# Performance work log

Measured on AMD Instinct MI355X. Metric: run time of the kernel, lower is better.

The kernel has to match this reference:

```python
import jax, jax.numpy as jnp
import numpy as np

# Module hyperparameters (init_kwargs)
OUTLINER_RATIO = 0.01
SUB_RATIO = 0.2
SUB_BIT = 8
RANK = 16


def setup_inputs() -> dict:
    key = jax.random.key(0)
    x = jax.random.normal(key, (8, 2048, 4096), dtype=jnp.float32)
    return {"x": x}


def _lowrank_approx(A, q, key):
    """Randomized rank-q approximation of A (torch.svd_lowrank style, niter=2).
    A: [N, D]. Returns Q @ (Q^T A), a rank-q approximation of A."""
    n = A.shape[1]
    omega = jax.random.normal(key, (n, q), dtype=A.dtype)
    Q, _ = jnp.linalg.qr(A @ omega)            # [N, q]
    for _ in range(2):                          # power iterations
        Q2, _ = jnp.linalg.qr(A.T @ Q)          # [D, q]
        Q, _ = jnp.linalg.qr(A @ Q2)            # [N, q]
    return Q @ (Q.T @ A)                        # [N, D], rank q


def _get_statistics(x):
    """Outlier threshold (1-ratio quantile of |x[0]|), top-norm column list,
    and per-tensor symmetric quantization scale for the sub-outlier columns."""
    ax0 = jnp.abs(x[0]).ravel()
    k = int(ax0.shape[0] * (1.0 - OUTLINER_RATIO))      # kthvalue, 1-indexed
    outliner = jnp.sort(ax0)[k - 1]
    col_norm = jnp.mean(jnp.abs(x), axis=(0, 1))        # [D] per-column mean |x|
    kcols = int(x.shape[-1] * SUB_RATIO)
    _, cols = jax.lax.top_k(col_norm, kcols)            # sub-outlier column ids
    col_mask = jnp.zeros((x.shape[-1],), bool).at[cols].set(True)
    x_rem = jnp.where(jnp.abs(x) > outliner, 0.0, x)    # remove outliers
    x_sub = jnp.where(col_mask, x_rem, 0.0)
    qmax = float(2 ** (SUB_BIT - 1) - 1)
    scale = jnp.max(jnp.abs(x_sub)) / qmax
    return outliner, cols, scale


def _compress(x, outliner, cols, scale):
    """fake_divide_outliner_suboutlinear_svd: split x into outliers (kept exact),
    sub-outlier columns (fake-quantized to SUB_BIT bits), and a rank-RANK
    approximation of the remainder; recombine."""
    shape = x.shape
    D = shape[-1]
    x_out = jnp.where(jnp.abs(x) > outliner, x, 0.0)
    x_rem = x - x_out
    col_mask = jnp.zeros((D,), bool).at[cols].set(True)
    x_sub = jnp.where(col_mask, x_rem, 0.0)
    x_rem2 = x_rem - x_sub
    qmax = 2 ** (SUB_BIT - 1) - 1
    x_sub_q = jnp.clip(jnp.round(x_sub / scale), -qmax - 1, qmax) * scale
    x_lr = _lowrank_approx(x_rem2.reshape(-1, D), RANK, jax.random.key(42))
    return x_lr.reshape(shape) + x_out + x_sub_q


def reference(x):
    # forward output of the module is exact-erf GELU (F.gelu default)
    result = jax.nn.gelu(x, approximate=False)
    # iteration=0 < 10: compute statistics and the compressed activation
    # that would be saved for backward (this is the custom-kernel-heavy path).
    outliner, cols, scale = _get_statistics(x)
    x_compressed = _compress(x, outliner, cols, scale)
    return result, x_compressed, outliner, scale
```

## Files before the change

### kernel.cpp

```cpp
#include <hip/hip_runtime.h>
#include <math.h>

#define D_   4096
#define N_   16384
#define TOT  67108864ULL
#define KSEL 8304721u

__device__ unsigned long long g_colsum[D_];
__device__ unsigned int  g_hist[2048];
__device__ unsigned int  g_state[2];
__device__ float         g_outliner;
__device__ unsigned int  g_maxbits;
__device__ float         g_scale;
__device__ unsigned char g_mask[D_];
__device__ float g_omega[D_ * 16];
__device__ float g_tall [N_ * 16];
__device__ float g_small[D_ * 16];
__device__ float g_part [16777216];
__device__ float g_gpart[64 * 256];
__device__ float g_M[256];

__device__ __forceinline__ unsigned rotl32(unsigned v, int s) { return (v << s) | (v >> (32 - s)); }

__device__ __forceinline__ float erfinv32(float xx) {
  float w = -log1pf(-xx * xx);
  float p;
  if (w < 5.f) {
    w -= 2.5f;
    p = 2.81022636e-08f;
    p = fmaf(p, w, 3.43273939e-07f);
    p = fmaf(p, w, -3.5233877e-06f);
    p = fmaf(p, w, -4.39150654e-06f);
    p = fmaf(p, w, 0.00021858087f);
    p = fmaf(p, w, -0.00125372503f);
    p = fmaf(p, w, -0.00417768164f);
    p = fmaf(p, w, 0.246640727f);
    p = fmaf(p, w, 1.50140941f);
  } else {
    w = sqrtf(w) - 3.f;
    p = -0.000200214257f;
    p = fmaf(p, w, 0.000100950558f);
    p = fmaf(p, w, 0.00134934322f);
    p = fmaf(p, w, -0.00367342844f);
    p = fmaf(p, w, 0.00573950773f);
    p = fmaf(p, w, -0.0076224613f);
    p = fmaf(p, w, 0.00943887047f);
    p = fmaf(p, w, 1.00167406f);
    p = fmaf(p, w, 2.83297682f);
  }
  return p * xx;
}

__device__ __forceinline__ float bits_to_normal(unsigned b) {
  float f = __uint_as_float((b >> 9) | 0x3f800000u) - 1.0f;
  float u = fmaf(f, 2.0f, -0.99999994f);
  u = fmaxf(-0.99999994f, u);
  return 1.41421356f * erfinv32(u);
}

__device__ __forceinline__ float gelu_exact(float v) {
  return 0.5f * v * (1.f + erff(v * 0.70710678f));
}

__global__ void k_init() {
  int t = threadIdx.x;
  for (int i = t; i < D_; i += 256) g_colsum[i] = 0ull;
  for (int i = t; i < 2048; i += 256) g_hist[i] = 0u;
  if (t == 0) { g_state[0] = KSEL; g_state[1] = 0u; g_maxbits = 0u; }
}

__global__ __launch_bounds__(256) void k_pass1(const float* __restrict__ x, float* __restrict__ out0) {
  __shared__ unsigned lh[4 * 2056];
  int t = threadIdx.x, b = blockIdx.x;
  bool doh = (b < 64);
  for (int i = t; i < 4 * 2056; i += 256) lh[i] = 0u;
  int cp = (t >> 6) * 2056;
  float acc[16];
#pragma unroll
  for (int j = 0; j < 16; ++j) acc[j] = 0.f;
  __syncthreads();
  const float4* xv = (const float4*)(x + (size_t)b * 131072);
  float4* ov = (float4*)(out0 + (size_t)b * 131072);
  for (int i = 0; i < 128; i += 4) {
#pragma unroll
    for (int jj = 0; jj < 4; ++jj) {
      int f = t + 256 * (i + jj);
      float4 v = xv[f];
      float4 g;
      g.x = gelu_exact(v.x); g.y = gelu_exact(v.y); g.z = gelu_exact(v.z); g.w = gelu_exact(v.w);
      ov[f] = g;
      acc[jj * 4 + 0] += fabsf(v.x);
      acc[jj * 4 + 1] += fabsf(v.y);
      acc[jj * 4 + 2] += fabsf(v.z);
      acc[jj * 4 + 3] += fabsf(v.w);
      if (doh) {
        atomicAdd(&lh[cp + ((__float_as_uint(v.x) & 0x7fffffffu) >> 21)], 1u);
        atomicAdd(&lh[cp + ((__float_as_uint(v.y) & 0x7fffffffu) >> 21)], 1u);
        atomicAdd(&lh[cp + ((__float_as_uint(v.z) & 0x7fffffffu) >> 21)], 1u);
        atomicAdd(&lh[cp + ((__float_as_uint(v.w) & 0x7fffffffu) >> 21)], 1u);
      }
    }
  }
#pragma unroll
  for (int jj = 0; jj < 4; ++jj) {
    int c4 = t + 256 * jj;
#pragma unroll
    for (int k = 0; k < 4; ++k) {
      unsigned long long q = (unsigned long long)((double)acc[jj * 4 + k] * 4294967296.0 + 0.5);
      atomicAdd(&g_colsum[4 * c4 + k], q);
    }
  }
  if (doh) {
    __syncthreads();
    for (int i = t; i < 2048; i += 256) {
      unsigned c = lh[i] + lh[2056 + i] + lh[4112 + i] + lh[6168 + i];
      if (c) atomicAdd(&g_hist[i], c);
    }
  }
}

__global__ __launch_bounds__(256) void k_histL(const float* __restrict__ x, int level) {
  __shared__ unsigned lh[2048];
  int t = threadIdx.x, b = blockIdx.x;
  for (int i = t; i < 2048; i += 256) lh[i] = 0u;
  __syncthreads();
  unsigned pre = g_state[1];
  const float4* xv = (const float4*)x;
  size_t base = (size_t)b * 16384;
  for (int i = 0; i < 64; ++i) {
    float4 v = xv[base + t + 256 * i];
    unsigned u;
#define HPROC(comp) \
    u = __float_as_uint(comp) & 0x7fffffffu; \
    if (level == 1) { if ((u >> 21) == (pre >> 21)) atomicAdd(&lh[(u >> 10) & 0x7ffu], 1u); } \
    else            { if ((u >> 10) == (pre >> 10)) atomicAdd(&lh[u & 0x3ffu], 1u); }
    HPROC(v.x) HPROC(v.y) HPROC(v.z) HPROC(v.w)
#undef HPROC
  }
  __syncthreads();
  for (int i = t; i < 2048; i += 256) { unsigned c = lh[i]; if (c) atomicAdd(&g_hist[i], c); }
}

__global__ void k_scan(int level, float* __restrict__ od) {
  __shared__ unsigned h[2048];
  __shared__ unsigned ps[256];
  int t = threadIdx.x;
  unsigned loc = 0;
#pragma unroll
  for (int i = 0; i < 8; ++i) { unsigned v = g_hist[t * 8 + i]; h[t * 8 + i] = v; loc += v; }
  ps[t] = loc;
  __syncthreads();
  if (t == 0) {
    unsigned krem = g_state[0], pre = g_state[1];
    unsigned cum = 0; int g = 0;
    for (; g < 255; ++g) { if (cum + ps[g] >= krem) break; cum += ps[g]; }
    int b = g * 8;
    for (; b < 2047; ++b) { if (cum + h[b] >= krem) break; cum += h[b]; }
    krem -= cum;
    if (level == 0)      pre = ((unsigned)b) << 21;
    else if (level == 1) pre |= ((unsigned)b) << 10;
    else { pre |= (unsigned)b; g_outliner = __uint_as_float(pre); od[0] = __uint_as_float(pre); }
    g_state[0] = krem; g_state[1] = pre;
  }
  __syncthreads();
  for (int i = t; i < 2048; i += 256) g_hist[i] = 0u;
}

__global__ __launch_bounds__(1024) void k_colsel() {
  __shared__ unsigned long long s[4096];
  int t = threadIdx.x;
  for (int m = 0; m < 4; ++m) s[t + 1024 * m] = g_colsum[t + 1024 * m];
  __syncthreads();
  for (int k = 2; k <= 4096; k <<= 1) {
    for (int j = k >> 1; j > 0; j >>= 1) {
#pragma unroll
      for (int m = 0; m < 4; ++m) {
        int i = t + 1024 * m;
        int l = i ^ j;
        if (l > i) {
          unsigned long long a = s[i], c = s[l];
          bool up = ((i & k) == 0);
          if (up ? (a > c) : (a < c)) { s[i] = c; s[l] = a; }
        }
      }
      __syncthreads();
    }
  }
  unsigned long long T = s[4096 - 819];
  for (int m = 0; m < 4; ++m) { int i = t + 1024 * m; g_mask[i] = (g_colsum[i] >= T) ? 1 : 0; }
}

__global__ void k_omega() {
  unsigned i = blockIdx.x * 256 + threadIdx.x;
  if (i >= 65536u) return;
  const unsigned ks0 = 0u, ks1 = 42u, ks2 = 0x1BD11BDAu ^ 42u;
  unsigned x0 = 0u + ks0;
  unsigned x1 = i  + ks1;
#define RND(r) { x0 += x1; x1 = rotl32(x1, r); x1 ^= x0; }
  RND(13) RND(15) RND(26) RND(6)   x0 += ks1; x1 += ks2 + 1u;
  RND(17) RND(29) RND(16) RND(24)  x0 += ks2; x1 += ks0 + 2u;
  RND(13) RND(15) RND(26) RND(6)   x0 += ks0; x1 += ks1 + 3u;
  RND(17) RND(29) RND(16) RND(24)  x0 += ks1; x1 += ks2 + 4u;
  RND(13) RND(15) RND(26) RND(6)   x0 += ks2; x1 += ks0 + 5u;
#undef RND
  g_omega[i] = bits_to_normal(x0 ^ x1);
}

__global__ __launch_bounds__(256) void k_AB(const float* __restrict__ x, int bsel) {
  __shared__ float xt[256 * 33];
  int t = threadIdx.x;
  int rb = blockIdx.x, ks = blockIdx.y;
  const float* Bm = bsel ? g_small : g_omega;
  float thr = g_outliner;
  float acc[16];
#pragma unroll
  for (int q = 0; q < 16; ++q) acc[q] = 0.f;
  int row0 = rb * 256;
  for (int ch = 0; ch < 8; ++ch) {
    int d0 = ks * 256 + ch * 32;
#pragma unroll
    for (int m = 0; m < 8; ++m) {
      int f = t + 256 * m;
      int r = f >> 3, c4 = f & 7;
      float4 v = *(const float4*)(x + (size_t)(row0 + r) * D_ + d0 + 4 * c4);
      uchar4 mk = *(const uchar4*)(g_mask + d0 + 4 * c4);
      float a0 = (mk.x || fabsf(v.x) > thr) ? 0.f : v.x;
      float a1 = (mk.y || fabsf(v.y) > thr) ? 0.f : v.y;
      float a2 = (mk.z || fabsf(v.z) > thr) ? 0.f : v.z;
      float a3 = (mk.w || fabsf(v.w) > thr) ? 0.f : v.w;
      int base = r * 33 + 4 * c4;
      xt[base + 0] = a0; xt[base + 1] = a1; xt[base + 2] = a2; xt[base + 3] = a3;
    }
    __syncthreads();
    for (int d = 0; d < 32; ++d) {
      const float* br = Bm + (size_t)(d0 + d) * 16;
      float a0 = xt[t * 33 + d];
#pragma unroll
      for (int q = 0; q < 16; ++q) acc[q] = fmaf(a0, br[q], acc[q]);
    }
    __syncthreads();
  }
  float* p0 = g_part + ((size_t)ks * N_ + row0 + t) * 16;
#pragma unroll
  for (int q4 = 0; q4 < 4; ++q4)
    *(float4*)(p0 + 4 * q4) = make_float4(acc[4*q4], acc[4*q4+1], acc[4*q4+2], acc[4*q4+3]);
}

__global__ __launch_bounds__(1024) void k_AtB(const float* __restrict__ x, int do_max) {
  __shared__ float wm[16];
  int t = threadIdx.x, b = blockIdx.x;
  float thr = g_outliner;
  uchar4 mk = *(const uchar4*)(g_mask + 4 * t);
  float acc[4][16];
#pragma unroll
  for (int j = 0; j < 4; ++j)
#pragma unroll
    for (int q = 0; q < 16; ++q) acc[j][q] = 0.f;
  float mx = 0.f;
  size_t row0 = (size_t)b * 64;
  for (int r = 0; r < 64; ++r) {
    size_t row = row0 + r;
    float4 v = *(const float4*)(x + row * D_ + 4 * t);
    const float* br = g_tall + row * 16;
    float ax = fabsf(v.x), ay = fabsf(v.y), az = fabsf(v.z), aw = fabsf(v.w);
    float a0 = (mk.x || ax > thr) ? 0.f : v.x;
    float a1 = (mk.y || ay > thr) ? 0.f : v.y;
    float a2 = (mk.z || az > thr) ? 0.f : v.z;
    float a3 = (mk.w || aw > thr) ? 0.f : v.w;
    if (do_max) {
      if (mk.x && ax <= thr) mx = fmaxf(mx, ax);
      if (mk.y && ay <= thr) mx = fmaxf(mx, ay);
      if (mk.z && az <= thr) mx = fmaxf(mx, az);
      if (mk.w && aw <= thr) mx = fmaxf(mx, aw);
    }
#pragma unroll
    for (int q = 0; q < 16; ++q) {
      float bq = br[q];
      acc[0][q] = fmaf(a0, bq, acc[0][q]);
      acc[1][q] = fmaf(a1, bq, acc[1][q]);
      acc[2][q] = fmaf(a2, bq, acc[2][q]);
      acc[3][q] = fmaf(a3, bq, acc[3][q]);
    }
  }
  float* pb = g_part + ((size_t)b * D_ + 4 * t) * 16;
#pragma unroll
  for (int j = 0; j < 4; ++j)
#pragma unroll
    for (int q4 = 0; q4 < 4; ++q4)
      *(float4*)(pb + j * 16 + 4 * q4) =
        make_float4(acc[j][4*q4], acc[j][4*q4+1], acc[j][4*q4+2], acc[j][4*q4+3]);
  if (do_max) {
#pragma unroll
    for (int off = 32; off > 0; off >>= 1) mx = fmaxf(mx, __shfl_xor(mx, off, 64));
    if ((t & 63) == 0) wm[t >> 6] = mx;
    __syncthreads();
    if (t == 0) {
      float m2 = wm[0];
      for (int i = 1; i < 16; ++i) m2 = fmaxf(m2, wm[i]);
      atomicMax(&g_maxbits, __float_as_uint(m2));
    }
  }
}

__global__ void k_scalewrite(float* __restrict__ od) {
  if (threadIdx.x == 0) {
    float s = __uint_as_float(g_maxbits) / 127.0f;
    g_scale = s; od[0] = s;
  }
}

__global__ __launch_bounds__(256) void k_combine(int mode) {
  int i = blockIdx.x * 256 + threadIdx.x;
  int np = mode ? 256 : 16;
  size_t stride4 = mode ? 16384 : 65536;
  float4* dst = mode ? (float4*)g_small : (float4*)g_tall;
  const float4* p = (const float4*)g_part;
  float4 s = make_float4(0.f, 0.f, 0.f, 0.f);
  for (int k2 = 0; k2 < np; ++k2) {
    float4 v = p[(size_t)k2 * stride4 + i];
    s.x += v.x; s.y += v.y; s.z += v.z; s.w += v.w;
  }
  dst[i] = s;
}

__global__ __launch_bounds__(256) void k_gram(int which) {
  __shared__ float ys[1024];
  const float* Y = which ? g_small : g_tall;
  int t = threadIdx.x;
  int i = t >> 4, j = t & 15;
  float acc = 0.f;
  size_t row0 = (size_t)blockIdx.x * 256;
  for (int c = 0; c < 4; ++c) {
    ((float4*)ys)[t] = *(const float4*)(Y + (row0 + c * 64) * 16 + 4 * t);
    __syncthreads();
    for (int r = 0; r < 64; ++r) acc = fmaf(ys[r * 16 + i], ys[r * 16 + j], acc);
    __syncthreads();
  }
  g_gpart[blockIdx.x * 256 + t] = acc;
}

__global__ void k_chol(int mode, int np) {
  __shared__ double G[256], L[256], M[256];
  int t = threadIdx.x;
  double s = 0.0;
  for (int p = 0; p < np; ++p) s += (double)g_gpart[p * 256 + t];
  G[t] = s; M[t] = 0.0; L[t] = 0.0;
  __syncthreads();
  for (int j = 0; j < 16; ++j) {
    if (t == j) {
      double d = G[j * 16 + j];
      for (int k = 0; k < j; ++k) d -= L[j * 16 + k] * L[j * 16 + k];
      L[j * 16 + j] = sqrt(d);
    }
    __syncthreads();
    if (t > j && t < 16) {
      double d = G[t * 16 + j];
      for (int k = 0; k < j; ++k) d -= L[t * 16 + k] * L[j * 16 + k];
      L[t * 16 + j] = d / L[j * 16 + j];
    }
    __syncthreads();
  }
  if (t < 16) {
    int jc = t;
    M[jc * 16 + jc] = 1.0 / L[jc * 16 + jc];
    for (int i2 = jc + 1; i2 < 16; ++i2) {
      double s2 = 0.0;
      for (int k = jc; k < i2; ++k) s2 += L[i2 * 16 + k] * M[k * 16 + jc];
      M[i2 * 16 + jc] = -s2 / L[i2 * 16 + i2];
    }
  }
  __syncthreads();
  if (mode == 0) g_M[t] = (float)M[t];
  else {
    int i2 = t >> 4, j2 = t & 15;
    double s2 = 0.0;
    for (int k = 0; k < 16; ++k) s2 += M[k * 16 + i2] * M[k * 16 + j2];
    g_M[t] = (float)s2;
  }
}

__global__ __launch_bounds__(256) void k_scaleQ(int which) {
  __shared__ float Mf[256];
  float* Y = which ? g_small : g_tall;
  int t = threadIdx.x;
  Mf[t] = g_M[t];
  __syncthreads();
  size_t row = (size_t)blockIdx.x * 256 + t;
  float4* yr = (float4*)(Y + row * 16);
  float4 v0 = yr[0], v1 = yr[1], v2 = yr[2], v3 = yr[3];
  float y[16] = {v0.x,v0.y,v0.z,v0.w, v1.x,v1.y,v1.z,v1.w, v2.x,v2.y,v2.z,v2.w, v3.x,v3.y,v3.z,v3.w};
  float q[16];
#pragma unroll
  for (int jq = 0; jq < 16; ++jq) {
    float s = 0.f;
    for (int iq = 0; iq <= jq; ++iq) s = fmaf(Mf[jq * 16 + iq], y[iq], s);
    q[jq] = s;
  }
  yr[0] = make_float4(q[0],q[1],q[2],q[3]);
  yr[1] = make_float4(q[4],q[5],q[6],q[7]);
  yr[2] = make_float4(q[8],q[9],q[10],q[11]);
  yr[3] = make_float4(q[12],q[13],q[14],q[15]);
}

__global__ __launch_bounds__(256) void k_Zsolve() {
  __shared__ float Gf[256];
  int t = threadIdx.x;
  Gf[t] = g_M[t];
  __syncthreads();
  size_t d = (size_t)blockIdx.x * 256 + t;
  float4* wr = (float4*)(g_small + d * 16);
  float4 v0 = wr[0], v1 = wr[1], v2 = wr[2], v3 = wr[3];
  float w[16] = {v0.x,v0.y,v0.z,v0.w, v1.x,v1.y,v1.z,v1.w, v2.x,v2.y,v2.z,v2.w, v3.x,v3.y,v3.z,v3.w};
  float z[16];
#pragma unroll
  for (int jq = 0; jq < 16; ++jq) {
    float s = 0.f;
#pragma unroll
    for (int iq = 0; iq < 16; ++iq) s = fmaf(Gf[jq * 16 + iq], w[iq], s);
    z[jq] = s;
  }
  wr[0] = make_float4(z[0],z[1],z[2],z[3]);
  wr[1] = make_float4(z[4],z[5],z[6],z[7]);
  wr[2] = make_float4(z[8],z[9],z[10],z[11]);
  wr[3] = make_float4(z[12],z[13],z[14],z[15]);
}

__global__ __launch_bounds__(256) void k_final(const float* __restrict__ x, float* __restrict__ out1) {
  __shared__ float zt[16 * 516];
  int t = threadIdx.x;
  int rb = blockIdx.x, pn = blockIdx.y;
  int d0 = pn * 512;
  int row0 = rb * 256;
#pragma unroll
  for (int i = 0; i < 8; ++i) {
    int f = t + 256 * i;
    int dd = f >> 2, q4 = f & 3;
    float4 zv = *(const float4*)(g_small + (size_t)(d0 + dd) * 16 + 4 * q4);
    zt[(4 * q4 + 0) * 516 + dd] = zv.x;
    zt[(4 * q4 + 1) * 516 + dd] = zv.y;
    zt[(4 * q4 + 2) * 516 + dd] = zv.z;
    zt[(4 * q4 + 3) * 516 + dd] = zv.w;
  }
  __syncthreads();
  float thr = g_outliner, sc = g_scale;
  int lf = t & 127;
  int half = t >> 7;
  int dl = 4 * lf;
  float4 zq[16];
#pragma unroll
  for (int q = 0; q < 16; ++q) zq[q] = *(const float4*)&zt[q * 516 + dl];
  uchar4 mk = *(const uchar4*)(g_mask + d0 + dl);
  for (int i = 0; i < 128; ++i) {
    int row = row0 + 2 * i + half;
    int rowu = __builtin_amdgcn_readfirstlane(row);
    const float* yr = g_tall + (size_t)rowu * 16;
    float4 v = *(const float4*)(x + (size_t)rowu * D_ + d0 + dl);
    float4 a = make_float4(0.f, 0.f, 0.f, 0.f);
#pragma unroll
    for (int q = 0; q < 16; ++q) {
      float yq = yr[q];
      a.x = fmaf(yq, zq[q].x, a.x); a.y = fmaf(yq, zq[q].y, a.y);
      a.z = fmaf(yq, zq[q].z, a.z); a.w = fmaf(yq, zq[q].w, a.w);
    }
    float4 o;
    o.x = a.x + (fabsf(v.x) > thr ? v.x : (mk.x ? fminf(fmaxf(rintf(v.x / sc), -128.f), 127.f) * sc : 0.f));
    o.y = a.y + (fabsf(v.y) > thr ? v.y : (mk.y ? fminf(fmaxf(rintf(v.y / sc), -128.f), 127.f) * sc : 0.f));
    o.z = a.z + (fabsf(v.z) > thr ? v.z : (mk.z ? fminf(fmaxf(rintf(v.z / sc), -128.f), 127.f) * sc : 0.f));
    o.w = a.w + (fabsf(v.w) > thr ? v.w : (mk.w ? fminf(fmaxf(rintf(v.w / sc), -128.f), 127.f) * sc : 0.f));
    *(float4*)(out1 + (size_t)rowu * D_ + d0 + dl) = o;
  }
}

extern "C" void kernel_launch(void* const* d_in, const int* in_sizes, int n_in,
                              void* d_out, int out_size, void* d_ws, size_t ws_size,
                              hipStream_t stream) {
  (void)in_sizes; (void)n_in; (void)out_size; (void)d_ws; (void)ws_size;
  const float* x = (const float*)d_in[0];
  float* out = (float*)d_out;
  float* out0    = out;
  float* out1    = out + TOT;
  float* o_outl  = out + 2 * TOT;
  float* o_scale = out + 2 * TOT + 1;

  hipLaunchKernelGGL(k_init,  dim3(1),   dim3(256), 0, stream);
  hipLaunchKernelGGL(k_pass1, dim3(512), dim3(256), 0, stream, x, out0);
  hipLaunchKernelGGL(k_scan,  dim3(1),   dim3(256), 0, stream, 0, o_outl);
  hipLaunchKernelGGL(k_histL, dim3(128), dim3(256), 0, stream, x, 1);
  hipLaunchKernelGGL(k_scan,  dim3(1),   dim3(256), 0, stream, 1, o_outl);
  hipLaunchKernelGGL(k_histL, dim3(128), dim3(256), 0, stream, x, 2);
  hipLaunchKernelGGL(k_scan,  dim3(1),   dim3(256), 0, stream, 2, o_outl);
  hipLaunchKernelGGL(k_colsel, dim3(1),  dim3(1024), 0, stream);
  hipLaunchKernelGGL(k_omega, dim3(256), dim3(256), 0, stream);
  hipLaunchKernelGGL(k_AB,      dim3(64, 16), dim3(256), 0, stream, x, 0);
  hipLaunchKernelGGL(k_combine, dim3(256),    dim3(256), 0, stream, 0);
  hipLaunchKernelGGL(k_gram,    dim3(64),     dim3(256), 0, stream, 0);
  hipLaunchKernelGGL(k_chol,    dim3(1),      dim3(256), 0, stream, 0, 64);
  hipLaunchKernelGGL(k_scaleQ,  dim3(64),     dim3(256), 0, stream, 0);
  hipLaunchKernelGGL(k_AtB,       dim3(256), dim3(1024), 0, stream, x, 1);
  hipLaunchKernelGGL(k_scalewrite, dim3(1),  dim3(64),   0, stream, o_scale);
  hipLaunchKernelGGL(k_combine,   dim3(64),  dim3(256),  0, stream, 1);
  hipLaunchKernelGGL(k_gram,      dim3(16),  dim3(256),  0, stream, 1);
  hipLaunchKernelGGL(k_chol,      dim3(1),   dim3(256),  0, stream, 0, 16);
  hipLaunchKernelGGL(k_scaleQ,    dim3(16),  dim3(256),  0, stream, 1);
  hipLaunchKernelGGL(k_AB,      dim3(64, 16), dim3(256), 0, stream, x, 1);
  hipLaunchKernelGGL(k_combine, dim3(256),    dim3(256), 0, stream, 0);
  hipLaunchKernelGGL(k_gram,    dim3(64),     dim3(256), 0, stream, 0);
  hipLaunchKernelGGL(k_chol,    dim3(1),      dim3(256), 0, stream, 0, 64);
  hipLaunchKernelGGL(k_scaleQ,  dim3(64),     dim3(256), 0, stream, 0);
  hipLaunchKernelGGL(k_AtB,     dim3(256), dim3(1024), 0, stream, x, 0);
  hipLaunchKernelGGL(k_combine, dim3(64),  dim3(256),  0, stream, 1);
  hipLaunchKernelGGL(k_gram,    dim3(16),  dim3(256),  0, stream, 1);
  hipLaunchKernelGGL(k_chol,    dim3(1),   dim3(256),  0, stream, 0, 16);
  hipLaunchKernelGGL(k_scaleQ,  dim3(16),  dim3(256),  0, stream, 1);
  hipLaunchKernelGGL(k_AB,      dim3(64, 16), dim3(256), 0, stream, x, 1);
  hipLaunchKernelGGL(k_combine, dim3(256),    dim3(256), 0, stream, 0);
  hipLaunchKernelGGL(k_gram,    dim3(64),     dim3(256), 0, stream, 0);
  hipLaunchKernelGGL(k_chol,    dim3(1),      dim3(256), 0, stream, 1, 64);
  hipLaunchKernelGGL(k_AtB,     dim3(256), dim3(1024), 0, stream, x, 0);
  hipLaunchKernelGGL(k_combine, dim3(64),  dim3(256),  0, stream, 1);
  hipLaunchKernelGGL(k_Zsolve,  dim3(16),  dim3(256),  0, stream);
  hipLaunchKernelGGL(k_final,   dim3(64, 8), dim3(256), 0, stream, x, out1);
}
```

Before: 1.290 ms.

## Reduce split-K partials in shared memory and drop global partial buffer

Restructures the tall-skinny A·B and Aᵀ·B kernels so each 1024-thread block handles a full reduction slice and sums partials in shared memory, writing the final result directly. This removes the 64 MB global partial buffer and the separate k_combine launches. k_AB now has each thread stream a 256-wide row segment from x, an uncoalesced access pattern across threads. k_AtB now reads 16 contiguous columns per row with scalar loads over 256 blocks, which may reduce bandwidth efficiency on x.

Measured after the change: 1.698 ms. 31.6% more time.

```diff
diff --git a/kernel.cpp b/kernel.cpp
--- a/kernel.cpp
+++ b/kernel.cpp
@@ -16,7 +16,6 @@
 __device__ float g_omega[D_ * 16];
 __device__ float g_tall [N_ * 16];
 __device__ float g_small[D_ * 16];
-__device__ float g_part [16777216];
 __device__ float g_gpart[64 * 256];
 __device__ float g_M[256];
 
@@ -206,99 +205,85 @@
   g_omega[i] = bits_to_normal(x0 ^ x1);
 }
 
-__global__ __launch_bounds__(256) void k_AB(const float* __restrict__ x, int bsel) {
-  __shared__ float xt[256 * 33];
-  int t = threadIdx.x;
-  int rb = blockIdx.x, ks = blockIdx.y;
+__global__ __launch_bounds__(1024) void k_AB(const float* __restrict__ x, int bsel) {
+  __shared__ float red[16 * 1024];
+  int t = threadIdx.x;
+  int r = t & 63, ks = t >> 6;
+  int row = blockIdx.x * 64 + r;
   const float* Bm = bsel ? g_small : g_omega;
   float thr = g_outliner;
   float acc[16];
 #pragma unroll
   for (int q = 0; q < 16; ++q) acc[q] = 0.f;
-  int row0 = rb * 256;
-  for (int ch = 0; ch < 8; ++ch) {
-    int d0 = ks * 256 + ch * 32;
-#pragma unroll
-    for (int m = 0; m < 8; ++m) {
-      int f = t + 256 * m;
-      int r = f >> 3, c4 = f & 7;
-      float4 v = *(const float4*)(x + (size_t)(row0 + r) * D_ + d0 + 4 * c4);
-      uchar4 mk = *(const uchar4*)(g_mask + d0 + 4 * c4);
-      float a0 = (mk.x || fabsf(v.x) > thr) ? 0.f : v.x;
-      float a1 = (mk.y || fabsf(v.y) > thr) ? 0.f : v.y;
-      float a2 = (mk.z || fabsf(v.z) > thr) ? 0.f : v.z;
-      float a3 = (mk.w || fabsf(v.w) > thr) ? 0.f : v.w;
-      int base = r * 33 + 4 * c4;
-      xt[base + 0] = a0; xt[base + 1] = a1; xt[base + 2] = a2; xt[base + 3] = a3;
-    }
-    __syncthreads();
-    for (int d = 0; d < 32; ++d) {
-      const float* br = Bm + (size_t)(d0 + d) * 16;
-      float a0 = xt[t * 33 + d];
-#pragma unroll
-      for (int q = 0; q < 16; ++q) acc[q] = fmaf(a0, br[q], acc[q]);
-    }
-    __syncthreads();
-  }
-  float* p0 = g_part + ((size_t)ks * N_ + row0 + t) * 16;
+  const float* xr = x + (size_t)row * D_ + ks * 256;
+  const unsigned char* mrow = g_mask + ks * 256;
+  const float* bb = Bm + (size_t)(ks * 256) * 16;
+  for (int j4 = 0; j4 < 64; ++j4) {
+    float4 v = *(const float4*)(xr + 4 * j4);
+    uchar4 mk = *(const uchar4*)(mrow + 4 * j4);
+    float a0 = (mk.x || fabsf(v.x) > thr) ? 0.f : v.x;
+    float a1 = (mk.y || fabsf(v.y) > thr) ? 0.f : v.y;
+    float a2 = (mk.z || fabsf(v.z) > thr) ? 0.f : v.z;
+    float a3 = (mk.w || fabsf(v.w) > thr) ? 0.f : v.w;
+    const float* b0 = bb + (size_t)(4 * j4) * 16;
+#pragma unroll
+    for (int q = 0; q < 16; ++q) {
+      float s = acc[q];
+      s = fmaf(a0, b0[q], s);
+      s = fmaf(a1, b0[16 + q], s);
+      s = fmaf(a2, b0[32 + q], s);
+      s = fmaf(a3, b0[48 + q], s);
+      acc[q] = s;
+    }
+  }
+  float* rp = red + ks * 1024 + r * 16;
 #pragma unroll
   for (int q4 = 0; q4 < 4; ++q4)
-    *(float4*)(p0 + 4 * q4) = make_float4(acc[4*q4], acc[4*q4+1], acc[4*q4+2], acc[4*q4+3]);
+    *(float4*)(rp + 4 * q4) = make_float4(acc[4*q4], acc[4*q4+1], acc[4*q4+2], acc[4*q4+3]);
+  __syncthreads();
+  int rr = t >> 4, qq = t & 15;
+  float s = 0.f;
+  for (int k2 = 0; k2 < 16; ++k2) s += red[k2 * 1024 + rr * 16 + qq];
+  g_tall[(size_t)(blockIdx.x * 64 + rr) * 16 + qq] = s;
 }
 
 __global__ __launch_bounds__(1024) void k_AtB(const float* __restrict__ x, int do_max) {
-  __shared__ float wm[16];
-  int t = threadIdx.x, b = blockIdx.x;
+  __shared__ float red[64 * 256];
+  int t = threadIdx.x;
+  int c = t & 15, rs = t >> 4;
+  int c0 = blockIdx.x * 16;
   float thr = g_outliner;
-  uchar4 mk = *(const uchar4*)(g_mask + 4 * t);
-  float acc[4][16];
-#pragma unroll
-  for (int j = 0; j < 4; ++j)
-#pragma unroll
-    for (int q = 0; q < 16; ++q) acc[j][q] = 0.f;
+  unsigned char mk = g_mask[c0 + c];
+  float acc[16];
+#pragma unroll
+  for (int q = 0; q < 16; ++q) acc[q] = 0.f;
   float mx = 0.f;
-  size_t row0 = (size_t)b * 64;
-  for (int r = 0; r < 64; ++r) {
-    size_t row = row0 + r;
-    float4 v = *(const float4*)(x + row * D_ + 4 * t);
+  size_t rowbase = (size_t)rs * 256;
+  for (int i = 0; i < 256; ++i) {
+    size_t row = rowbase + i;
+    float v = x[row * D_ + c0 + c];
+    float av = fabsf(v);
+    float a = (mk || av > thr) ? 0.f : v;
+    if (do_max) { if (mk && av <= thr) mx = fmaxf(mx, av); }
     const float* br = g_tall + row * 16;
-    float ax = fabsf(v.x), ay = fabsf(v.y), az = fabsf(v.z), aw = fabsf(v.w);
-    float a0 = (mk.x || ax > thr) ? 0.f : v.x;
-    float a1 = (mk.y || ay > thr) ? 0.f : v.y;
-    float a2 = (mk.z || az > thr) ? 0.f : v.z;
-    float a3 = (mk.w || aw > thr) ? 0.f : v.w;
-    if (do_max) {
-      if (mk.x && ax <= thr) mx = fmaxf(mx, ax);
-      if (mk.y && ay <= thr) mx = fmaxf(mx, ay);
-      if (mk.z && az <= thr) mx = fmaxf(mx, az);
-      if (mk.w && aw <= thr) mx = fmaxf(mx, aw);
-    }
-#pragma unroll
-    for (int q = 0; q < 16; ++q) {
-      float bq = br[q];
-      acc[0][q] = fmaf(a0, bq, acc[0][q]);
-      acc[1][q] = fmaf(a1, bq, acc[1][q]);
-      acc[2][q] = fmaf(a2, bq, acc[2][q]);
-      acc[3][q] = fmaf(a3, bq, acc[3][q]);
-    }
-  }
-  float* pb = g_part + ((size_t)b * D_ + 4 * t) * 16;
-#pragma unroll
-  for (int j = 0; j < 4; ++j)
-#pragma unroll
-    for (int q4 = 0; q4 < 4; ++q4)
-      *(float4*)(pb + j * 16 + 4 * q4) =
-        make_float4(acc[j][4*q4], acc[j][4*q4+1], acc[j][4*q4+2], acc[j][4*q4+3]);
+#pragma unroll
+    for (int q = 0; q < 16; ++q) acc[q] = fmaf(a, br[q], acc[q]);
+  }
+  float* rp = red + rs * 256 + c * 16;
+#pragma unroll
+  for (int q4 = 0; q4 < 4; ++q4)
+    *(float4*)(rp + 4 * q4) = make_float4(acc[4*q4], acc[4*q4+1], acc[4*q4+2], acc[4*q4+3]);
   if (do_max) {
 #pragma unroll
     for (int off = 32; off > 0; off >>= 1) mx = fmaxf(mx, __shfl_xor(mx, off, 64));
-    if ((t & 63) == 0) wm[t >> 6] = mx;
-    __syncthreads();
-    if (t == 0) {
-      float m2 = wm[0];
-      for (int i = 1; i < 16; ++i) m2 = fmaxf(m2, wm[i]);
-      atomicMax(&g_maxbits, __float_as_uint(m2));
-    }
+    if ((t & 63) == 0) atomicMax(&g_maxbits, __float_as_uint(mx));
+  }
+  __syncthreads();
+  if (t < 256) {
+    int c2 = t >> 4, q2 = t & 15;
+    float s = 0.f;
+    for (int k2 = 0; k2 < 64; ++k2) s += red[k2 * 256 + c2 * 16 + q2];
+    g_small[(size_t)(c0 + c2) * 16 + q2] = s;
   }
 }
 
@@ -307,20 +292,6 @@
     float s = __uint_as_float(g_maxbits) / 127.0f;
     g_scale = s; od[0] = s;
   }
-}
-
-__global__ __launch_bounds__(256) void k_combine(int mode) {
-  int i = blockIdx.x * 256 + threadIdx.x;
-  int np = mode ? 256 : 16;
-  size_t stride4 = mode ? 16384 : 65536;
-  float4* dst = mode ? (float4*)g_small : (float4*)g_tall;
-  const float4* p = (const float4*)g_part;
-  float4 s = make_float4(0.f, 0.f, 0.f, 0.f);
-  for (int k2 = 0; k2 < np; ++k2) {
-    float4 v = p[(size_t)k2 * stride4 + i];
-    s.x += v.x; s.y += v.y; s.z += v.z; s.w += v.w;
-  }
-  dst[i] = s;
 }
 
 __global__ __launch_bounds__(256) void k_gram(int which) {
@@ -491,33 +462,27 @@
   hipLaunchKernelGGL(k_scan,  dim3(1),   dim3(256), 0, stream, 2, o_outl);
   hipLaunchKernelGGL(k_colsel, dim3(1),  dim3(1024), 0, stream);
   hipLaunchKernelGGL(k_omega, dim3(256), dim3(256), 0, stream);
-  hipLaunchKernelGGL(k_AB,      dim3(64, 16), dim3(256), 0, stream, x, 0);
-  hipLaunchKernelGGL(k_combine, dim3(256),    dim3(256), 0, stream, 0);
-  hipLaunchKernelGGL(k_gram,    dim3(64),     dim3(256), 0, stream, 0);
-  hipLaunchKernelGGL(k_chol,    dim3(1),      dim3(256), 0, stream, 0, 64);
-  hipLaunchKernelGGL(k_scaleQ,  dim3(64),     dim3(256), 0, stream, 0);
+  hipLaunchKernelGGL(k_AB,     dim3(256), dim3(1024), 0, stream, x, 0);
+  hipLaunchKernelGGL(k_gram,   dim3(64),  dim3(256),  0, stream, 0);
+  hipLaunchKernelGGL(k_chol,   dim3(1),   dim3(256),  0, stream, 0, 64);
+  hipLaunchKernelGGL(k_scaleQ, dim3(64),  dim3(256),  0, stream, 0);
   hipLaunchKernelGGL(k_AtB,       dim3(256), dim3(1024), 0, stream, x, 1);
   hipLaunchKernelGGL(k_scalewrite, dim3(1),  dim3(64),   0, stream, o_scale);
-  hipLaunchKernelGGL(k_combine,   dim3(64),  dim3(256),  0, stream, 1);
   hipLaunchKernelGGL(k_gram,      dim3(16),  dim3(256),  0, stream, 1);
   hipLaunchKernelGGL(k_chol,      dim3(1),   dim3(256),  0, stream, 0, 16);
   hipLaunchKernelGGL(k_scaleQ,    dim3(16),  dim3(256),  0, stream, 1);
-  hipLaunchKernelGGL(k_AB,      dim3(64, 16), dim3(256), 0, stream, x, 1);
-  hipLaunchKernelGGL(k_combine, dim3(256),    dim3(256), 0, stream, 0);
-  hipLaunchKernelGGL(k_gram,    dim3(64),     dim3(256), 0, stream, 0);
-  hipLaunchKernelGGL(k_chol,    dim3(1),      dim3(256), 0, stream, 0, 64);
-  hipLaunchKernelGGL(k_scaleQ,  dim3(64),     dim3(256), 0, stream, 0);
-  hipLaunchKernelGGL(k_AtB,     dim3(256), dim3(1024), 0, stream, x, 0);
-  hipLaunchKernelGGL(k_combine, dim3(64),  dim3(256),  0, stream, 1);
-  hipLaunchKernelGGL(k_gram,    dim3(16),  dim3(256),  0, stream, 1);
-  hipLaunchKernelGGL(k_chol,    dim3(1),   dim3(256),  0, stream, 0, 16);
-  hipLaunchKernelGGL(k_scaleQ,  dim3(16),  dim3(256),  0, stream, 1);
-  hipLaunchKernelGGL(k_AB,      dim3(64, 16), dim3(256), 0, stream, x, 1);
-  hipLaunchKernelGGL(k_combine, dim3(256),    dim3(256), 0, stream, 0);
-  hipLaunchKernelGGL(k_gram,    dim3(64),     dim3(256), 0, stream, 0);
-  hipLaunchKernelGGL(k_chol,    dim3(1),      dim3(256), 0, stream, 1, 64);
-  hipLaunchKernelGGL(k_AtB,     dim3(256), dim3(1024), 0, stream, x, 0);
-  hipLaunchKernelGGL(k_combine, dim3(64),  dim3(256),  0, stream, 1);
-  hipLaunchKernelGGL(k_Zsolve,  dim3(16),  dim3(256),  0, stream);
-  hipLaunchKernelGGL(k_final,   dim3(64, 8), dim3(256), 0, stream, x, out1);
-}
+  hipLaunchKernelGGL(k_AB,     dim3(256), dim3(1024), 0, stream, x, 1);
+  hipLaunchKernelGGL(k_gram,   dim3(64),  dim3(256),  0, stream, 0);
+  hipLaunchKernelGGL(k_chol,   dim3(1),   dim3(256),  0, stream, 0, 64);
+  hipLaunchKernelGGL(k_scaleQ, dim3(64),  dim3(256),  0, stream, 0);
+  hipLaunchKernelGGL(k_AtB,    dim3(256), dim3(1024), 0, stream, x, 0);
+  hipLaunchKernelGGL(k_gram,   dim3(16),  dim3(256),  0, stream, 1);
+  hipLaunchKernelGGL(k_chol,   dim3(1),   dim3(256),  0, stream, 0, 16);
+  hipLaunchKernelGGL(k_scaleQ, dim3(16),  dim3(256),  0, stream, 1);
+  hipLaunchKernelGGL(k_AB,     dim3(256), dim3(1024), 0, stream, x, 1);
+  hipLaunchKernelGGL(k_gram,   dim3(64),  dim3(256),  0, stream, 0);
+  hipLaunchKernelGGL(k_chol,   dim3(1),   dim3(256),  0, stream, 1, 64);
+  hipLaunchKernelGGL(k_AtB,    dim3(256), dim3(1024), 0, stream, x, 0);
+  hipLaunchKernelGGL(k_Zsolve, dim3(16),  dim3(256),  0, stream);
+  hipLaunchKernelGGL(k_final,  dim3(64, 8), dim3(256), 0, stream, x, out1);
+}
```
